# Kernel tuning notes

Measured on AMD Instinct MI355X. Metric: run time of the kernel, lower is better.

Reference implementation:

```python
import jax, jax.numpy as jnp
import numpy as np

EMBED_DIM = 1024
NUM_HEADS = 16
HEAD_WIDTH = 64  # EMBED_DIM == NUM_HEADS * HEAD_WIDTH
B, L = 2, 1024


def setup_inputs() -> dict:
    key = jax.random.key(0)
    ks = jax.random.split(key, 7)
    s = EMBED_DIM ** -0.5
    return {
        "x": jax.random.normal(ks[0], (B, L, EMBED_DIM), dtype=jnp.float32),
        "bias": jax.random.normal(ks[1], (B, L, L, NUM_HEADS), dtype=jnp.float32),
        # nn.Linear weights are (out_features, in_features)
        "w_proj": jax.random.normal(ks[2], (3 * EMBED_DIM, EMBED_DIM), dtype=jnp.float32) * s,
        "w_o": jax.random.normal(ks[3], (EMBED_DIM, EMBED_DIM), dtype=jnp.float32) * s,
        "b_o": jnp.zeros((EMBED_DIM,), dtype=jnp.float32),
        "w_g": jax.random.normal(ks[4], (EMBED_DIM, EMBED_DIM), dtype=jnp.float32) * s,
        "b_g": jnp.ones((EMBED_DIM,), dtype=jnp.float32),
    }


def reference(x, bias, w_proj, w_o, b_o, w_g, b_g):
    b, l, e = x.shape
    h, hw = NUM_HEADS, HEAD_WIDTH
    # fused QKV projection: (B,L,3E) -> (B,H,L,3*hw), head-major split as in torch
    t = jnp.einsum('ble,fe->blf', x, w_proj)
    t = t.reshape(b, l, h, 3 * hw).transpose(0, 2, 1, 3)  # (B,H,L,3hw)
    q, k, v = jnp.split(t, 3, axis=-1)
    q = q * (hw ** -0.5)
    a = jnp.einsum('bhqc,bhkc->bhqk', q, k)
    a = a + bias.transpose(0, 3, 1, 2)  # bias: (B,Lq,Lk,H) -> (B,H,Lq,Lk)
    a = jax.nn.softmax(a, axis=-1)
    y = jnp.einsum('bhqk,bhkc->bqhc', a, v).reshape(b, l, e)
    g = jax.nn.sigmoid(jnp.einsum('ble,fe->blf', x, w_g) + b_g)
    y = g * y
    y = jnp.einsum('ble,fe->blf', y, w_o) + b_o
    # faithful to original rearrange('... lq lk h -> ... h lq lk') applied to (B,h,lq,lk):
    attn = jnp.transpose(a, (0, 3, 1, 2))  # (B, lk, h, lq)
    return y, attn
```

## Files before the change

### kernel.cpp

```cpp
#include <hip/hip_runtime.h>
#include <hip/hip_bf16.h>
#include <stdint.h>

typedef __attribute__((ext_vector_type(4))) float f32x4;
typedef __attribute__((ext_vector_type(8))) short short8;
typedef __attribute__((ext_vector_type(4))) unsigned short u16x4;
typedef unsigned short us;

#define DEV __device__ __forceinline__
#define MFMA16(a, b, c) __builtin_amdgcn_mfma_f32_16x16x32_bf16(a, b, c, 0, 0, 0)

DEV us f2b(float x) {
  union { float f; uint32_t u; } c; c.f = x;
  uint32_t r = (c.u + 0x7fffu + ((c.u >> 16) & 1u)) >> 16;
  return (us)r;
}
DEV float b2f(us x) {
  union { uint32_t u; float f; } c; c.u = ((uint32_t)x) << 16;
  return c.f;
}
DEV us f2h(float x) { union { _Float16 h; us u; } c; c.h = (_Float16)x; return c.u; }
DEV float h2f(us x) { union { us u; _Float16 h; } c; c.u = x; return (float)c.h; }

DEV void gload_lds16(const void* g, void* l) {
  __builtin_amdgcn_global_load_lds((const __attribute__((address_space(1))) void*)g,
                                   (__attribute__((address_space(3))) void*)l, 16, 0, 0);
}

__global__ __launch_bounds__(256) void prep_k(
    const float* __restrict__ x, const float* __restrict__ wproj,
    const float* __restrict__ wg, const float* __restrict__ wo,
    us* __restrict__ Xbf, us* __restrict__ Wbf, us* __restrict__ Wobf) {
  int i = blockIdx.x * 256 + threadIdx.x;
  const float* src; us* dst;
  if (i < 524288)               { src = x     + (size_t)i * 4;                  dst = Xbf + (size_t)i * 4; }
  else if (i < 524288 + 786432) { int j = i - 524288;            src = wproj + (size_t)j * 4; dst = Wbf + (size_t)j * 4; }
  else if (i < 524288 + 786432 + 262144) { int j = i - (524288 + 786432); src = wg + (size_t)j * 4; dst = Wbf + 3145728 + (size_t)j * 4; }
  else                          { int j = i - (524288 + 786432 + 262144); src = wo + (size_t)j * 4; dst = Wobf + (size_t)j * 4; }
  f32x4 v = *(const f32x4*)src;
  u16x4 o; o.x = f2b(v.x); o.y = f2b(v.y); o.z = f2b(v.z); o.w = f2b(v.w);
  *(u16x4*)dst = o;
}

DEV void gemm_stage(char* sm, const us* A, const us* Bw,
                    int tileMrow, int tileNrow, int buf, int kt, int lane, int wid) {
  const char* gA = (const char*)A;
  const char* gB = (const char*)Bw;
#pragma unroll
  for (int i = 0; i < 2; ++i) {
    int c = wid * 2 + i;
    int off = c * 1024 + lane * 16;
    int r = off >> 6, cb = off & 63;
    gload_lds16(gA + ((size_t)(tileMrow + r) * 2048) + kt * 64 + cb, sm + buf * 8192 + c * 1024);
    gload_lds16(gB + ((size_t)(tileNrow + r) * 2048) + kt * 64 + cb, sm + 16384 + buf * 8192 + c * 1024);
  }
}

DEV void gemm_main(const us* A, const us* Bw,
                   int tileMrow, int tileNrow, f32x4 acc[4][4], char* sm) {
  int tid = threadIdx.x, lane = tid & 63, wid = tid >> 6;
  int wr = wid >> 1, wc = wid & 1;
  gemm_stage(sm, A, Bw, tileMrow, tileNrow, 0, 0, lane, wid);
  for (int kt = 0; kt < 32; ++kt) {
    __syncthreads();
    if (kt < 31) gemm_stage(sm, A, Bw, tileMrow, tileNrow, (kt + 1) & 1, kt + 1, lane, wid);
    int ab = (kt & 1) * 8192;
    int rb = (lane & 15) * 64 + ((lane >> 4) * 16);
    short8 af[4], bf[4];
#pragma unroll
    for (int mi = 0; mi < 4; ++mi)
      af[mi] = *(const short8*)(sm + ab + (wr * 64 + mi * 16) * 64 + rb);
#pragma unroll
    for (int ni = 0; ni < 4; ++ni)
      bf[ni] = *(const short8*)(sm + 16384 + ab + (wc * 64 + ni * 16) * 64 + rb);
#pragma unroll
    for (int mi = 0; mi < 4; ++mi)
#pragma unroll
      for (int ni = 0; ni < 4; ++ni)
        acc[mi][ni] = MFMA16(af[mi], bf[ni], acc[mi][ni]);
  }
}

__global__ __launch_bounds__(256) void gemm_qkvg_k(
    const us* __restrict__ Xbf, const us* __restrict__ Wbf,
    us* __restrict__ Qb, us* __restrict__ Kb, us* __restrict__ Vt,
    float* __restrict__ G, const float* __restrict__ bg) {
  __shared__ char sm[32768];
  int bid = blockIdx.x;
  int swz = (bid & 7) * 64 + (bid >> 3);
  int tileM = swz >> 5, tileN = swz & 31;
  f32x4 acc[4][4] = {};
  gemm_main(Xbf, Wbf, tileM * 128, tileN * 128, acc, sm);
  int lane = threadIdx.x & 63, wid = threadIdx.x >> 6;
  int wr = wid >> 1, wc = wid & 1;
#pragma unroll
  for (int mi = 0; mi < 4; ++mi)
#pragma unroll
    for (int ni = 0; ni < 4; ++ni)
#pragma unroll
      for (int j = 0; j < 4; ++j) {
        int row = tileM * 128 + wr * 64 + mi * 16 + ((lane >> 4) << 2) + j;
        int col = tileN * 128 + wc * 64 + ni * 16 + (lane & 15);
        float v = acc[mi][ni][j];
        int b = row >> 10, l = row & 1023;
        if (col < 3072) {
          int h = col / 192, r = col - h * 192;
          size_t base = ((size_t)(b * 16 + h) * 1024 + l) * 64;
          if (r < 64)        Qb[base + r] = f2b(v * 0.125f);
          else if (r < 128)  Kb[base + (r - 64)] = f2b(v);
          else               Vt[((size_t)(b * 16 + h) * 64 + (r - 128)) * 1024 + l] = f2b(v);
        } else {
          int e = col - 3072;
          float s = v + bg[e];
          G[(size_t)row * 1024 + e] = 1.f / (1.f + __expf(-s));
        }
      }
}

__global__ __launch_bounds__(256) void qk_k(
    const us* __restrict__ Qb, const us* __restrict__ Kb, us* __restrict__ SE) {
  int tid = threadIdx.x, lane = tid & 63, w = tid >> 6;
  int la = lane & 15, lg = lane >> 4;
  int bid = blockIdx.x;
  int g = bid >> 8, qt = (bid >> 3) & 31, xx = bid & 7;
  int bh = g * 8 + xx;
  int b = bh >> 4, h = bh & 15;
  int qb = qt * 32;
  const us* Qh = Qb + (size_t)bh * 65536;
  const us* Kh = Kb + (size_t)bh * 65536;
  int lk0 = w * 256;

  short8 qf[2][2];
#pragma unroll
  for (int qh = 0; qh < 2; ++qh)
#pragma unroll
    for (int ks = 0; ks < 2; ++ks)
      qf[qh][ks] = *(const short8*)(Qh + (size_t)(qb + qh * 16 + la) * 64 + ks * 32 + lg * 8);

  f32x4 acc[2][16] = {};
#pragma unroll
  for (int nf = 0; nf < 16; ++nf) {
    const us* kr = Kh + (size_t)(lk0 + nf * 16 + la) * 64 + lg * 8;
    short8 kf0 = *(const short8*)kr;
    short8 kf1 = *(const short8*)(kr + 32);
    acc[0][nf] = MFMA16(kf0, qf[0][0], acc[0][nf]);
    acc[0][nf] = MFMA16(kf1, qf[0][1], acc[0][nf]);
    acc[1][nf] = MFMA16(kf0, qf[1][0], acc[1][nf]);
    acc[1][nf] = MFMA16(kf1, qf[1][1], acc[1][nf]);
  }
#pragma unroll
  for (int qh = 0; qh < 2; ++qh)
#pragma unroll
    for (int nf = 0; nf < 16; ++nf) {
      u16x4 o;
#pragma unroll
      for (int j = 0; j < 4; ++j) o[j] = f2h(acc[qh][nf][j]);
      *(u16x4*)(SE + (((size_t)(b * 1024 + qb + qh * 16 + la) * 16 + h) << 10) +
                lk0 + nf * 16 + lg * 4) = o;
    }
}

__global__ __launch_bounds__(256) void exp_k(
    us* __restrict__ SE, const float* __restrict__ bias, float* __restrict__ linv) {
  __shared__ float bt[4352];
  int tid = threadIdx.x;
  int la = tid & 15, h = tid >> 4;
  int bid = blockIdx.x;
  int lq = bid & 1023, b = bid >> 10;
  const float* brow = bias + ((size_t)b << 24) + ((size_t)lq << 14);
  us* row = SE + (((size_t)(b * 1024 + lq) * 16 + h) << 10);
  float lsum = 0.f;

#pragma unroll 1
  for (int ch = 0; ch < 4; ++ch) {
    int lk0 = ch * 256;
    __syncthreads();
#pragma unroll
    for (int i = 0; i < 4; ++i) {
      int f = i * 256 + tid;
      int lk = f >> 2, h4 = f & 3;
      f32x4 v = *(const f32x4*)(brow + (size_t)(lk0 + lk) * 16 + h4 * 4);
      int base = lk * 17 + h4 * 4;
      bt[base] = v.x; bt[base + 1] = v.y; bt[base + 2] = v.z; bt[base + 3] = v.w;
    }
    __syncthreads();
#pragma unroll
    for (int j = 0; j < 4; ++j) {
      int lkl = 4 * (la + 16 * j);
      u16x4 sv = *(const u16x4*)(row + lk0 + lkl);
      u16x4 ev;
#pragma unroll
      for (int i = 0; i < 4; ++i) {
        float e = __expf(h2f(sv[i]) + bt[(lkl + i) * 17 + h]);
        lsum += e;
        ev[i] = f2b(e);
      }
      *(u16x4*)(row + lk0 + lkl) = ev;
    }
  }
#pragma unroll
  for (int d = 1; d < 16; d <<= 1) lsum += __shfl_xor(lsum, d);
  if (la == 0) linv[((size_t)(b * 16 + h) << 10) + lq] = 1.f / lsum;
}

__global__ __launch_bounds__(256) void pv_k(
    const us* __restrict__ E, const us* __restrict__ Vt,
    const float* __restrict__ linv, const float* __restrict__ G,
    float* __restrict__ outa, us* __restrict__ Ybf) {
  __shared__ char sm[49792];
  float* lv = (float*)(sm + 49664);
  int tid = threadIdx.x, lane = tid & 63, w = tid >> 6;
  int la = lane & 15, lg = lane >> 4;
  int bid = blockIdx.x;
  int g = bid >> 8, qt = (bid >> 3) & 31, xx = bid & 7;
  int bh = g * 8 + xx;
  int b = bh >> 4, h = bh & 15;
  int qb = qt * 32;
  if (tid < 32) lv[tid] = linv[((size_t)bh << 10) + qb + tid];
  __syncthreads();
  char* pb = sm + w * 4096;
  const us* Vh = Vt + (size_t)bh * 65536;
  f32x4 yacc[2][4] = {};
  int lkw = w * 256;

#pragma unroll 1
  for (int cc = 0; cc < 4; ++cc) {
    int lk0 = lkw + cc * 64;
#pragma unroll
    for (int it = 0; it < 4; ++it) {
      int ci = it * 64 + lane;
      int q = ci >> 3, c16 = ci & 7;
      short8 ev = *(const short8*)(E + (((size_t)(b * 1024 + qb + q) * 16 + h) << 10) + lk0 + c16 * 8);
      *(short8*)(pb + q * 128 + ((c16 * 16) ^ ((q & 7) << 4))) = ev;
    }
#pragma unroll
    for (int it = 0; it < 8; ++it) {
      int idx = it * 64 + lane;
      int lkL = idx >> 3, q4 = idx & 7;
      f32x4 ov;
#pragma unroll
      for (int i = 0; i < 4; ++i) {
        int q = q4 * 4 + i;
        us e = *(const us*)(pb + q * 128 + ((2 * lkL) ^ ((q & 7) << 4)));
        ov[i] = b2f(e) * lv[q];
      }
      *(f32x4*)(outa + (((size_t)(b * 1024 + lk0 + lkL) * 16 + h) << 10) + qb + q4 * 4) = ov;
    }
#pragma unroll
    for (int ks = 0; ks < 2; ++ks) {
      short8 pa[2];
#pragma unroll
      for (int qh = 0; qh < 2; ++qh) {
        int row = qh * 16 + la;
        pa[qh] = *(const short8*)(pb + row * 128 + ((ks * 64 + lg * 16) ^ ((row & 7) << 4)));
      }
#pragma unroll
      for (int ni = 0; ni < 4; ++ni) {
        short8 vf = *(const short8*)(Vh + (size_t)(ni * 16 + la) * 1024 + lk0 + ks * 32 + lg * 8);
        yacc[0][ni] = MFMA16(pa[0], vf, yacc[0][ni]);
        yacc[1][ni] = MFMA16(pa[1], vf, yacc[1][ni]);
      }
    }
  }

  float* red = (float*)(sm + 16384);
#pragma unroll
  for (int qh = 0; qh < 2; ++qh)
#pragma unroll
    for (int ni = 0; ni < 4; ++ni)
#pragma unroll
      for (int j = 0; j < 4; ++j) {
        int r = qh * 16 + lg * 4 + j, c = ni * 16 + la;
        red[w * 2080 + r * 65 + c] = yacc[qh][ni][j];
      }
  __syncthreads();
#pragma unroll
  for (int rr = 0; rr < 8; ++rr) {
    int e = rr * 256 + tid;
    int r = e >> 6, c = e & 63;
    float s = red[r * 65 + c] + red[2080 + r * 65 + c] +
              red[4160 + r * 65 + c] + red[6240 + r * 65 + c];
    size_t gi = (((size_t)(b * 1024 + qb + r)) << 10) + h * 64 + c;
    Ybf[gi] = f2b(s * lv[r] * G[gi]);
  }
}

__global__ __launch_bounds__(256) void gemm_out_k(
    const us* __restrict__ Ybf, const us* __restrict__ Wobf,
    const float* __restrict__ bo, float* __restrict__ outy) {
  __shared__ char sm[32768];
  int bid = blockIdx.x;
  int swz = (bid & 7) * 16 + (bid >> 3);
  int tileM = swz >> 3, tileN = swz & 7;
  f32x4 acc[4][4] = {};
  gemm_main(Ybf, Wobf, tileM * 128, tileN * 128, acc, sm);
  int lane = threadIdx.x & 63, wid = threadIdx.x >> 6;
  int wr = wid >> 1, wc = wid & 1;
#pragma unroll
  for (int mi = 0; mi < 4; ++mi)
#pragma unroll
    for (int ni = 0; ni < 4; ++ni)
#pragma unroll
      for (int j = 0; j < 4; ++j) {
        int row = tileM * 128 + wr * 64 + mi * 16 + ((lane >> 4) << 2) + j;
        int col = tileN * 128 + wc * 64 + ni * 16 + (lane & 15);
        outy[(size_t)row * 1024 + col] = acc[mi][ni][j] + bo[col];
      }
}

extern "C" void kernel_launch(void* const* d_in, const int* in_sizes, int n_in,
                              void* d_out, int out_size, void* d_ws, size_t ws_size,
                              hipStream_t stream) {
  const float* x     = (const float*)d_in[0];
  const float* bias  = (const float*)d_in[1];
  const float* wproj = (const float*)d_in[2];
  const float* wo    = (const float*)d_in[3];
  const float* bo    = (const float*)d_in[4];
  const float* wg    = (const float*)d_in[5];
  const float* bg    = (const float*)d_in[6];
  float* outy = (float*)d_out;
  float* outa = outy + 2097152;

  char* ws = (char*)d_ws;
  us*    Xbf  = (us*)(ws);
  us*    Wbf  = (us*)(ws + 4  * 1024 * 1024);
  us*    Wobf = (us*)(ws + 12 * 1024 * 1024);
  us*    Qb   = (us*)(ws + 14 * 1024 * 1024);
  us*    Kb   = (us*)(ws + 18 * 1024 * 1024);
  us*    Vt   = (us*)(ws + 22 * 1024 * 1024);
  float* G    = (float*)(ws + 26 * 1024 * 1024);
  us*    Ybf  = (us*)(ws + 34 * 1024 * 1024);
  us*    SE   = (us*)(ws + (size_t)38 * 1024 * 1024);
  float* linv = (float*)(ws + (size_t)102 * 1024 * 1024);
  if (ws_size < (size_t)103 * 1024 * 1024) return;

  prep_k<<<dim3(7168), dim3(256), 0, stream>>>(x, wproj, wg, wo, Xbf, Wbf, Wobf);
  gemm_qkvg_k<<<dim3(512), dim3(256), 0, stream>>>(Xbf, Wbf, Qb, Kb, Vt, G, bg);
  qk_k<<<dim3(1024), dim3(256), 0, stream>>>(Qb, Kb, SE);
  exp_k<<<dim3(2048), dim3(256), 0, stream>>>(SE, bias, linv);
  pv_k<<<dim3(1024), dim3(256), 0, stream>>>(SE, Vt, linv, G, outa, Ybf);
  gemm_out_k<<<dim3(128), dim3(256), 0, stream>>>(Ybf, Wobf, bo, outy);
}
```

Before: 209.7 us.

## Fuse QK scores, bias add and exp into one kernel with partial row sums

Merges the QK^T kernel and the bias+exp kernel into one kernel. Each block covers 16 queries, a 256-key chunk and all 16 heads, and double-buffers bias tiles through shared memory. The bias is loaded into the MFMA accumulator as its initial value, then exp is applied and bf16 probabilities are written directly. This removes the fp16 score round trip through global memory. Per-chunk row sums go to a partial buffer that the PV kernel adds up, so that kernel does a little more work and the exp runs with no max subtraction, as it did before.

```diff
diff --git a/kernel.cpp b/kernel.cpp
--- a/kernel.cpp
+++ b/kernel.cpp
@@ -19,8 +19,6 @@
   union { uint32_t u; float f; } c; c.u = ((uint32_t)x) << 16;
   return c.f;
 }
-DEV us f2h(float x) { union { _Float16 h; us u; } c; c.h = (_Float16)x; return c.u; }
-DEV float h2f(us x) { union { us u; _Float16 h; } c; c.u = x; return (float)c.h; }
 
 DEV void gload_lds16(const void* g, void* l) {
   __builtin_amdgcn_global_load_lds((const __attribute__((address_space(1))) void*)g,
@@ -117,95 +115,94 @@
       }
 }
 
-__global__ __launch_bounds__(256) void qk_k(
-    const us* __restrict__ Qb, const us* __restrict__ Kb, us* __restrict__ SE) {
+__global__ __launch_bounds__(512, 4) void qke_k(
+    const us* __restrict__ Qb, const us* __restrict__ Kb,
+    const float* __restrict__ bias, us* __restrict__ E,
+    float* __restrict__ lpart) {
+  __shared__ float bt[2][8704];
   int tid = threadIdx.x, lane = tid & 63, w = tid >> 6;
   int la = lane & 15, lg = lane >> 4;
   int bid = blockIdx.x;
-  int g = bid >> 8, qt = (bid >> 3) & 31, xx = bid & 7;
-  int bh = g * 8 + xx;
-  int b = bh >> 4, h = bh & 15;
-  int qb = qt * 32;
-  const us* Qh = Qb + (size_t)bh * 65536;
-  const us* Kh = Kb + (size_t)bh * 65536;
-  int lk0 = w * 256;
+  int grp = bid & 7, qt = bid >> 3;
+  int b = grp >> 2, kc = grp & 3;
+  int lq0 = qt * 16, lk00 = kc * 256;
+  int h0 = w * 2;
 
   short8 qf[2][2];
 #pragma unroll
-  for (int qh = 0; qh < 2; ++qh)
+  for (int t = 0; t < 2; ++t) {
+    size_t bh = (size_t)(b * 16 + h0 + t);
 #pragma unroll
     for (int ks = 0; ks < 2; ++ks)
-      qf[qh][ks] = *(const short8*)(Qh + (size_t)(qb + qh * 16 + la) * 64 + ks * 32 + lg * 8);
-
-  f32x4 acc[2][16] = {};
-#pragma unroll
-  for (int nf = 0; nf < 16; ++nf) {
-    const us* kr = Kh + (size_t)(lk0 + nf * 16 + la) * 64 + lg * 8;
-    short8 kf0 = *(const short8*)kr;
-    short8 kf1 = *(const short8*)(kr + 32);
-    acc[0][nf] = MFMA16(kf0, qf[0][0], acc[0][nf]);
-    acc[0][nf] = MFMA16(kf1, qf[0][1], acc[0][nf]);
-    acc[1][nf] = MFMA16(kf0, qf[1][0], acc[1][nf]);
-    acc[1][nf] = MFMA16(kf1, qf[1][1], acc[1][nf]);
-  }
-#pragma unroll
-  for (int qh = 0; qh < 2; ++qh)
-#pragma unroll
-    for (int nf = 0; nf < 16; ++nf) {
-      u16x4 o;
-#pragma unroll
-      for (int j = 0; j < 4; ++j) o[j] = f2h(acc[qh][nf][j]);
-      *(u16x4*)(SE + (((size_t)(b * 1024 + qb + qh * 16 + la) * 16 + h) << 10) +
-                lk0 + nf * 16 + lg * 4) = o;
-    }
-}
-
-__global__ __launch_bounds__(256) void exp_k(
-    us* __restrict__ SE, const float* __restrict__ bias, float* __restrict__ linv) {
-  __shared__ float bt[4352];
-  int tid = threadIdx.x;
-  int la = tid & 15, h = tid >> 4;
-  int bid = blockIdx.x;
-  int lq = bid & 1023, b = bid >> 10;
-  const float* brow = bias + ((size_t)b << 24) + ((size_t)lq << 14);
-  us* row = SE + (((size_t)(b * 1024 + lq) * 16 + h) << 10);
-  float lsum = 0.f;
-
+      qf[t][ks] = *(const short8*)(Qb + bh * 65536 + (size_t)(lq0 + la) * 64 + ks * 32 + lg * 8);
+  }
+
+  const float* bsrc = bias + ((size_t)b << 24) + ((size_t)lq0 << 14);
+#pragma unroll
+  for (int i = 0; i < 4; ++i) {
+    int f = i * 512 + tid;
+    int h4 = f & 3, lk = (f >> 2) & 31, q = f >> 7;
+    f32x4 v = *(const f32x4*)(bsrc + ((size_t)q << 14) + ((size_t)(lk00 + lk) << 4) + h4 * 4);
+    float* d = &bt[0][(q * 32 + lk) * 17 + h4 * 4];
+    d[0] = v.x; d[1] = v.y; d[2] = v.z; d[3] = v.w;
+  }
+
+  float lacc[2] = {0.f, 0.f};
 #pragma unroll 1
-  for (int ch = 0; ch < 4; ++ch) {
-    int lk0 = ch * 256;
+  for (int sc = 0; sc < 8; ++sc) {
     __syncthreads();
-#pragma unroll
-    for (int i = 0; i < 4; ++i) {
-      int f = i * 256 + tid;
-      int lk = f >> 2, h4 = f & 3;
-      f32x4 v = *(const f32x4*)(brow + (size_t)(lk0 + lk) * 16 + h4 * 4);
-      int base = lk * 17 + h4 * 4;
-      bt[base] = v.x; bt[base + 1] = v.y; bt[base + 2] = v.z; bt[base + 3] = v.w;
-    }
-    __syncthreads();
-#pragma unroll
-    for (int j = 0; j < 4; ++j) {
-      int lkl = 4 * (la + 16 * j);
-      u16x4 sv = *(const u16x4*)(row + lk0 + lkl);
-      u16x4 ev;
+    if (sc < 7) {
+      int lkg2 = lk00 + (sc + 1) * 32;
+      float* bd = bt[(sc + 1) & 1];
 #pragma unroll
       for (int i = 0; i < 4; ++i) {
-        float e = __expf(h2f(sv[i]) + bt[(lkl + i) * 17 + h]);
-        lsum += e;
-        ev[i] = f2b(e);
-      }
-      *(u16x4*)(row + lk0 + lkl) = ev;
-    }
-  }
-#pragma unroll
-  for (int d = 1; d < 16; d <<= 1) lsum += __shfl_xor(lsum, d);
-  if (la == 0) linv[((size_t)(b * 16 + h) << 10) + lq] = 1.f / lsum;
+        int f = i * 512 + tid;
+        int h4 = f & 3, lk = (f >> 2) & 31, q = f >> 7;
+        f32x4 v = *(const f32x4*)(bsrc + ((size_t)q << 14) + ((size_t)(lkg2 + lk) << 4) + h4 * 4);
+        float* d = &bd[(q * 32 + lk) * 17 + h4 * 4];
+        d[0] = v.x; d[1] = v.y; d[2] = v.z; d[3] = v.w;
+      }
+    }
+    const float* btc = bt[sc & 1];
+    int lkg = lk00 + sc * 32;
+#pragma unroll
+    for (int t = 0; t < 2; ++t) {
+      int h = h0 + t;
+      const us* Kh = Kb + (size_t)(b * 16 + h) * 65536;
+#pragma unroll
+      for (int fr = 0; fr < 2; ++fr) {
+        const us* kr = Kh + (size_t)(lkg + fr * 16 + la) * 64 + lg * 8;
+        short8 kf0 = *(const short8*)kr;
+        short8 kf1 = *(const short8*)(kr + 32);
+        f32x4 a;
+#pragma unroll
+        for (int j = 0; j < 4; ++j)
+          a[j] = btc[(la * 32 + fr * 16 + lg * 4 + j) * 17 + h];
+        a = MFMA16(kf0, qf[t][0], a);
+        a = MFMA16(kf1, qf[t][1], a);
+        u16x4 ev;
+#pragma unroll
+        for (int j = 0; j < 4; ++j) {
+          float e = __expf(a[j]);
+          lacc[t] += e;
+          ev[j] = f2b(e);
+        }
+        *(u16x4*)(E + (((size_t)(b * 1024 + lq0 + la) * 16 + h) << 10) + lkg + fr * 16 + lg * 4) = ev;
+      }
+    }
+  }
+#pragma unroll
+  for (int t = 0; t < 2; ++t) {
+    float s = lacc[t];
+    s += __shfl_xor(s, 16);
+    s += __shfl_xor(s, 32);
+    if (lg == 0) lpart[kc * 32768 + (b * 16 + h0 + t) * 1024 + lq0 + la] = s;
+  }
 }
 
 __global__ __launch_bounds__(256) void pv_k(
     const us* __restrict__ E, const us* __restrict__ Vt,
-    const float* __restrict__ linv, const float* __restrict__ G,
+    const float* __restrict__ lpart, const float* __restrict__ G,
     float* __restrict__ outa, us* __restrict__ Ybf) {
   __shared__ char sm[49792];
   float* lv = (float*)(sm + 49664);
@@ -216,7 +213,11 @@
   int bh = g * 8 + xx;
   int b = bh >> 4, h = bh & 15;
   int qb = qt * 32;
-  if (tid < 32) lv[tid] = linv[((size_t)bh << 10) + qb + tid];
+  if (tid < 32) {
+    int r = bh * 1024 + qb + tid;
+    float s = lpart[r] + lpart[32768 + r] + lpart[65536 + r] + lpart[98304 + r];
+    lv[tid] = 1.f / s;
+  }
   __syncthreads();
   char* pb = sm + w * 4096;
   const us* Vh = Vt + (size_t)bh * 65536;
@@ -330,14 +331,13 @@
   us*    Vt   = (us*)(ws + 22 * 1024 * 1024);
   float* G    = (float*)(ws + 26 * 1024 * 1024);
   us*    Ybf  = (us*)(ws + 34 * 1024 * 1024);
-  us*    SE   = (us*)(ws + (size_t)38 * 1024 * 1024);
-  float* linv = (float*)(ws + (size_t)102 * 1024 * 1024);
-  if (ws_size < (size_t)103 * 1024 * 1024) return;
+  float* lpart= (float*)(ws + (size_t)38 * 1024 * 1024);
+  us*    E    = (us*)   (ws + (size_t)40 * 1024 * 1024);
+  if (ws_size < (size_t)104 * 1024 * 1024) return;
 
   prep_k<<<dim3(7168), dim3(256), 0, stream>>>(x, wproj, wg, wo, Xbf, Wbf, Wobf);
   gemm_qkvg_k<<<dim3(512), dim3(256), 0, stream>>>(Xbf, Wbf, Qb, Kb, Vt, G, bg);
-  qk_k<<<dim3(1024), dim3(256), 0, stream>>>(Qb, Kb, SE);
-  exp_k<<<dim3(2048), dim3(256), 0, stream>>>(SE, bias, linv);
-  pv_k<<<dim3(1024), dim3(256), 0, stream>>>(SE, Vt, linv, G, outa, Ybf);
+  qke_k<<<dim3(512), dim3(512), 0, stream>>>(Qb, Kb, bias, E, lpart);
+  pv_k<<<dim3(1024), dim3(256), 0, stream>>>(E, Vt, lpart, G, outa, Ybf);
   gemm_out_k<<<dim3(128), dim3(256), 0, stream>>>(Ybf, Wobf, bo, outy);
 }
```

After: 203.2 us. 3.1% less time.
